# Performance work log

Measured on AMD Instinct MI355X. Metric: run time of the kernel, lower is better.

The kernel has to match this reference:

```python
import jax, jax.numpy as jnp
import numpy as np

LAG = 5
MSG_HID = 256
N_ATOMS = 30
N_EDGES = N_ATOMS * (N_ATOMS - 1)  # 870
BATCH = 2
T = 200


def _rel_matrices():
    # fully-connected directed graph, no self loops (standard NRI encoding)
    recv, send = [], []
    for i in range(N_ATOMS):
        for j in range(N_ATOMS):
            if i != j:
                recv.append(i)
                send.append(j)
    rel_rec = np.zeros((N_EDGES, N_ATOMS), dtype=np.float32)
    rel_send = np.zeros((N_EDGES, N_ATOMS), dtype=np.float32)
    rel_rec[np.arange(N_EDGES), recv] = 1.0
    rel_send[np.arange(N_EDGES), send] = 1.0
    return jnp.asarray(rel_rec), jnp.asarray(rel_send)


def setup_inputs() -> dict:
    key = jax.random.key(0)
    ks = jax.random.split(key, 14)
    rel_rec, rel_send = _rel_matrices()
    s = 0.05
    return {
        "inputs": jax.random.normal(ks[0], (BATCH, N_ATOMS, T), jnp.float32),
        "mu": jax.random.normal(ks[1], (BATCH, N_EDGES), jnp.float32),
        "logvar": jax.random.normal(ks[2], (BATCH, N_EDGES), jnp.float32) * 0.1,
        "eps": jax.random.normal(ks[3], (BATCH, N_EDGES), jnp.float32),
        "rel_rec": rel_rec,
        "rel_send": rel_send,
        "w_msg1": jax.random.normal(ks[4], (2 * LAG, MSG_HID), jnp.float32) * s,
        "b_msg1": jnp.zeros((MSG_HID,), jnp.float32),
        "w_msg2": jax.random.normal(ks[5], (MSG_HID, MSG_HID), jnp.float32) * s,
        "b_msg2": jnp.zeros((MSG_HID,), jnp.float32),
        "w_out1": jax.random.normal(ks[6], (LAG + MSG_HID, MSG_HID), jnp.float32) * s,
        "b_out1": jnp.zeros((MSG_HID,), jnp.float32),
        "w_out2": jax.random.normal(ks[7], (MSG_HID, MSG_HID), jnp.float32) * s,
        "b_out2": jnp.zeros((MSG_HID,), jnp.float32),
        "w_out3": jax.random.normal(ks[8], (MSG_HID, 1), jnp.float32) * s,
        "b_out3": jnp.zeros((1,), jnp.float32),
    }


def reference(inputs, mu, logvar, eps, rel_rec, rel_send,
              w_msg1, b_msg1, w_msg2, b_msg2,
              w_out1, b_out1, w_out2, b_out2, w_out3, b_out3):
    # reparametrize: edges [B, E]
    edges = eps * jnp.exp(0.5 * logvar) + mu

    # lag-stack: data [B, T-lag, N, lag]
    Tm = inputs.shape[2] - LAG
    data = jnp.stack([inputs[:, :, i:i + Tm] for i in range(LAG)], axis=-1)
    data = jnp.transpose(data, (0, 2, 1, 3))  # [B, Tm, N, lag]

    # gather node features to edges via one-hot matmuls
    receivers = jnp.einsum('en,btnl->btel', rel_rec, data)   # [B, Tm, E, lag]
    senders = jnp.einsum('en,btnl->btel', rel_send, data)    # [B, Tm, E, lag]
    pre_msg = jnp.concatenate([senders, receivers], axis=-1)  # [B, Tm, E, 2*lag]

    msg = jax.nn.relu(pre_msg @ w_msg1 + b_msg1)
    msg = jax.nn.relu(msg @ w_msg2 + b_msg2)                 # [B, Tm, E, hid]
    msg = msg * edges[:, None, :, None]                       # edge mask

    # scatter-aggregate messages back to receiver nodes
    agg_msgs = jnp.einsum('bteh,en->btnh', msg, rel_rec)      # [B, Tm, N, hid]

    aug = jnp.concatenate([data, agg_msgs], axis=-1)          # [B, Tm, N, lag+hid]
    pred = jax.nn.relu(aug @ w_out1 + b_out1)
    pred = jax.nn.relu(pred @ w_out2 + b_out2)
    pred = (pred @ w_out3 + b_out3)[..., 0]                   # [B, Tm, N]

    return jnp.transpose(pred, (0, 2, 1))                     # [B, N, Tm]
```

## Files before the change

kernel.cpp:

```cpp
#include <hip/hip_runtime.h>

#define LAG 5
#define HID 256
#define NA 30
#define NE 870
#define TM 195
#define TT 200
#define NB 2
#define EPN 29
#define TB2 98
#define NROWS (NB * TM * NA)
#define APAD 4
#define KC 32
#define UVSLABS (NB * TM)
#define W2F_ELEMS (HID * HID)
#define W1F_ELEMS (HID * 288)
#define NWG2 (NB * NA * TB2)
#define Q8 (NWG2 / 8)

typedef _Float16 f16;
typedef _Float16 f16x8 __attribute__((ext_vector_type(8)));
typedef float floatx4 __attribute__((ext_vector_type(4)));
typedef float floatx16 __attribute__((ext_vector_type(16)));

__global__ __launch_bounds__(256) void k1_prep(
    const float* __restrict__ inputs, const float* __restrict__ w_msg1,
    const float* __restrict__ b_msg1, const float* __restrict__ w_msg2,
    const float* __restrict__ w_out1, const float* __restrict__ w_out2,
    f16* __restrict__ u, f16* __restrict__ v, f16* __restrict__ w2frag,
    f16* __restrict__ w1frag, f16* __restrict__ w2ofrag)
{
    const int bid = blockIdx.x, tid = threadIdx.x;
    if (bid < UVSLABS) {
        __shared__ float w1_lds[10 * 256];
        __shared__ float b1_lds[256];
        __shared__ float feats[30 * 5];
        const int b = bid / TM, t = bid % TM;
        #pragma unroll
        for (int i = 0; i < 10; ++i) w1_lds[i * 256 + tid] = w_msg1[i * 256 + tid];
        b1_lds[tid] = b_msg1[tid];
        if (tid < 150) {
            const int n = tid / 5, l = tid % 5;
            feats[tid] = inputs[(b * NA + n) * TT + t + l];
        }
        __syncthreads();
        if (tid < 240) {
            const int n = tid >> 3;
            float fr[LAG];
            #pragma unroll
            for (int l = 0; l < LAG; ++l) fr[l] = feats[n * 5 + l];
            const int slab = (b * TM + t) * (32 * 240);
            #pragma unroll 4
            for (int c = 0; c < 32; ++c) {
                const int col = c * 8 + (tid & 7);
                float ua = b1_lds[col], va = 0.f;
                #pragma unroll
                for (int l = 0; l < LAG; ++l) {
                    ua = fmaf(fr[l], w1_lds[l * 256 + col], ua);
                    va = fmaf(fr[l], w1_lds[(LAG + l) * 256 + col], va);
                }
                u[slab + c * 240 + tid] = (f16)ua;
                v[slab + c * 240 + tid] = (f16)va;
            }
        }
    } else if (bid < UVSLABS + 32) {
        const int fidx = (bid - UVSLABS) * 256 + tid;
        const int lane = fidx & 63;
        const int kc = (fidx >> 6) & 15;
        const int c32 = fidx >> 10;
        const int col = c32 * 32 + (lane & 31);
        const int kb = kc * 16 + (lane >> 5) * 8;
        f16x8 vv;
        #pragma unroll
        for (int x = 0; x < 8; ++x) vv[x] = (f16)w_msg2[(kb + x) * HID + col];
        *(f16x8*)&w2frag[fidx * 8] = vv;
    } else if (bid < UVSLABS + 32 + 36) {
        const int fidx = (bid - (UVSLABS + 32)) * 256 + tid;
        const int lane = fidx & 63;
        const int kc = (fidx >> 6) % 9;
        const int ntc = fidx / (64 * 9);
        const int col = ntc * 16 + (lane & 15);
        const int kb = kc * KC + (lane >> 4) * 8;
        f16x8 vv;
        #pragma unroll
        for (int x = 0; x < 8; ++x) {
            const int k = kb + x;
            float val;
            if (k < 256)      val = w_out1[(5 + k) * HID + col];
            else if (k < 261) val = w_out1[(k - 256) * HID + col];
            else              val = 0.f;
            vv[x] = (f16)val;
        }
        *(f16x8*)&w1frag[fidx * 8] = vv;
    } else {
        const int fidx = (bid - (UVSLABS + 32 + 36)) * 256 + tid;
        const int lane = fidx & 63;
        const int kc = (fidx >> 6) & 7;
        const int ntc = fidx >> 9;
        const int col = ntc * 16 + (lane & 15);
        const int kb = kc * KC + (lane >> 4) * 8;
        f16x8 vv;
        #pragma unroll
        for (int x = 0; x < 8; ++x) vv[x] = (f16)w_out2[(kb + x) * HID + col];
        *(f16x8*)&w2ofrag[fidx * 8] = vv;
    }
}

__global__ __launch_bounds__(256, 4) void k2_msg(
    const f16* __restrict__ u, const f16* __restrict__ v,
    const f16* __restrict__ w2frag,
    const float* __restrict__ mu, const float* __restrict__ logvar,
    const float* __restrict__ eps, const float* __restrict__ b_msg2,
    f16* __restrict__ agg)
{
    __shared__ f16 a_lds[32 * 64 * 8];
    __shared__ float ev_lds[32];

    const int bid0 = blockIdx.x;
    const int bid = (bid0 & 7) * Q8 + (bid0 >> 3);

    const int n  = bid % NA;
    const int tb = (bid / NA) % TB2;
    const int b  = bid / (NA * TB2);
    const int t0 = tb * 2;
    const int tid = threadIdx.x;
    const int lane = tid & 63, w = tid >> 6;
    const int h = lane >> 5, l31 = lane & 31;

    if (tid < 32) {
        float evv = 0.f;
        if (tid < EPN) {
            const int e = b * NE + n * EPN + tid;
            evv = eps[e] * __expf(0.5f * logvar[e]) + mu[e];
        }
        ev_lds[tid] = evv;
    }

    const f16x8 z8 = {(f16)0, (f16)0, (f16)0, (f16)0, (f16)0, (f16)0, (f16)0, (f16)0};

    auto stage_iter = [&](int i) {
        const int task = i * 256 + tid;
        const int frag = task >> 6, fl = task & 63;
        const int tt = frag >> 4, kcs = frag & 15;
        const int hh = fl >> 5, ei = fl & 31;
        const int c = kcs * 2 + hh;
        const int t = t0 + tt;
        f16x8 out8 = z8;
        if (ei < EPN && t < TM) {
            const int rowbase = ((b * TM + t) * 32 + c) * 240;
            const int j = ei + (ei >= n);
            const f16x8 uu = *(const f16x8*)(u + rowbase + j * 8);
            const f16x8 vv = *(const f16x8*)(v + rowbase + n * 8);
            out8 = __builtin_elementwise_max(uu + vv, z8);
        }
        *(f16x8*)&a_lds[task * 8] = out8;
    };

    #pragma unroll
    for (int s = 0; s < 4; ++s) stage_iter(s < 2 ? s : s + 2);

    const f16* bb[2];
    bb[0] = w2frag + (((2 * w + 0) * 16) << 9) + (lane << 3);
    bb[1] = w2frag + (((2 * w + 1) * 16) << 9) + (lane << 3);
    f16x8 b0[2], b1[2];
    #pragma unroll
    for (int nt = 0; nt < 2; ++nt) {
        b0[nt] = *(const f16x8*)(bb[nt] + (0 << 9));
        b1[nt] = *(const f16x8*)(bb[nt] + (1 << 9));
    }

    floatx16 acc[2][2];
    #pragma unroll
    for (int tt = 0; tt < 2; ++tt)
        #pragma unroll
        for (int nt = 0; nt < 2; ++nt)
            #pragma unroll
            for (int x = 0; x < 16; ++x) acc[tt][nt][x] = 0.f;

    __syncthreads();

    #pragma unroll
    for (int kc = 0; kc < 8; ++kc) {
        f16x8 b2[2];
        #pragma unroll
        for (int nt = 0; nt < 2; ++nt)
            b2[nt] = *(const f16x8*)(bb[nt] + ((kc + 2) << 9));
        f16x8 af[2];
        #pragma unroll
        for (int tt = 0; tt < 2; ++tt)
            af[tt] = *(const f16x8*)&a_lds[((tt * 16 + kc) * 64 + lane) * 8];
        __builtin_amdgcn_s_setprio(1);
        #pragma unroll
        for (int nt = 0; nt < 2; ++nt)
            #pragma unroll
            for (int tt = 0; tt < 2; ++tt)
                acc[tt][nt] = __builtin_amdgcn_mfma_f32_32x32x16_f16(af[tt], b0[nt], acc[tt][nt], 0, 0, 0);
        __builtin_amdgcn_s_setprio(0);
        #pragma unroll
        for (int nt = 0; nt < 2; ++nt) { b0[nt] = b1[nt]; b1[nt] = b2[nt]; }
        if ((kc & 1) == 0) {
            const int half = kc >> 1;
            stage_iter(half < 2 ? half + 2 : half + 4);
        }
    }

    __syncthreads();

    #pragma unroll
    for (int kc = 8; kc < 16; ++kc) {
        f16x8 b2[2];
        #pragma unroll
        for (int nt = 0; nt < 2; ++nt) {
            b2[nt] = b1[nt];
            if (kc < 14) b2[nt] = *(const f16x8*)(bb[nt] + ((kc + 2) << 9));
        }
        f16x8 af[2];
        #pragma unroll
        for (int tt = 0; tt < 2; ++tt)
            af[tt] = *(const f16x8*)&a_lds[((tt * 16 + kc) * 64 + lane) * 8];
        __builtin_amdgcn_s_setprio(1);
        #pragma unroll
        for (int nt = 0; nt < 2; ++nt)
            #pragma unroll
            for (int tt = 0; tt < 2; ++tt)
                acc[tt][nt] = __builtin_amdgcn_mfma_f32_32x32x16_f16(af[tt], b0[nt], acc[tt][nt], 0, 0, 0);
        __builtin_amdgcn_s_setprio(0);
        #pragma unroll
        for (int nt = 0; nt < 2; ++nt) { b0[nt] = b1[nt]; b1[nt] = b2[nt]; }
    }

    float evr[16];
    #pragma unroll
    for (int reg = 0; reg < 16; ++reg)
        evr[reg] = ev_lds[(reg & 3) + 8 * (reg >> 2) + 4 * h];
    float b2s[2];
    #pragma unroll
    for (int nt = 0; nt < 2; ++nt) b2s[nt] = b_msg2[(2 * w + nt) * 32 + l31];

    #pragma unroll
    for (int tt = 0; tt < 2; ++tt) {
        const int t = t0 + tt;
        #pragma unroll
        for (int nt = 0; nt < 2; ++nt) {
            float part = 0.f;
            #pragma unroll
            for (int reg = 0; reg < 16; ++reg)
                part += evr[reg] * fmaxf(acc[tt][nt][reg] + b2s[nt], 0.f);
            part += __shfl_xor(part, 32, 64);
            if (h == 0 && t < TM)
                agg[(((b * TM + t) * NA + n) << 8) + (2 * w + nt) * 32 + l31] = (f16)part;
        }
    }
}

__global__ __launch_bounds__(256) void k3_out(
    const f16* __restrict__ agg, const float* __restrict__ inputs,
    const f16* __restrict__ w1frag, const f16* __restrict__ w2ofrag,
    const float* __restrict__ b_out1, const float* __restrict__ b_out2,
    const float* __restrict__ w_out3, const float* __restrict__ b_out3,
    float* __restrict__ out)
{
    __shared__ f16 a1[32][288 + APAD];
    __shared__ float red[4][32];

    const int R0 = blockIdx.x * 32;
    const int tid = threadIdx.x;
    const int lane = tid & 63, w = tid >> 6;
    const int q = lane >> 4, m15 = lane & 15;
    const int wbase = w * 64;

    #pragma unroll
    for (int i = 0; i < 4; ++i) {
        const int task = i * 256 + tid;
        const int row = task >> 5, c = task & 31;
        const int R = R0 + row;
        f16x8 val;
        if (R < NROWS) {
            val = *(const f16x8*)&agg[(R << 8) + c * 8];
        } else {
            for (int x = 0; x < 8; ++x) val[x] = (f16)0.f;
        }
        *(f16x8*)&a1[row][c * 8] = val;
    }
    if (tid < 32) {
        const int R = R0 + tid;
        if (R < NROWS) {
            const int b = R / (TM * NA), rem = R % (TM * NA);
            const int t = rem / NA, n = rem % NA;
            const float* ip = inputs + (b * NA + n) * TT + t;
            #pragma unroll
            for (int l = 0; l < LAG; ++l) a1[tid][256 + l] = (f16)ip[l];
            #pragma unroll
            for (int k = 261; k < 288; ++k) a1[tid][k] = (f16)0.f;
        } else {
            for (int k = 256; k < 288; ++k) a1[tid][k] = (f16)0.f;
        }
    }

    floatx4 acc[2][4];
    #pragma unroll
    for (int ms = 0; ms < 2; ++ms)
        #pragma unroll
        for (int nt = 0; nt < 4; ++nt) acc[ms][nt] = (floatx4){0.f, 0.f, 0.f, 0.f};

    const f16* b1base = w1frag + (lane << 3);
    f16x8 bcur[4], bnxt[4];
    #pragma unroll
    for (int nt = 0; nt < 4; ++nt)
        bcur[nt] = *(const f16x8*)(b1base + (((w * 4 + nt) * 9 + 0) << 9));

    __syncthreads();

    #pragma unroll
    for (int kc = 0; kc < 9; ++kc) {
        if (kc < 8) {
            #pragma unroll
            for (int nt = 0; nt < 4; ++nt)
                bnxt[nt] = *(const f16x8*)(b1base + (((w * 4 + nt) * 9 + kc + 1) << 9));
        }
        f16x8 af[2];
        #pragma unroll
        for (int ms = 0; ms < 2; ++ms)
            af[ms] = *(const f16x8*)&a1[ms * 16 + m15][kc * KC + q * 8];
        #pragma unroll
        for (int nt = 0; nt < 4; ++nt)
            #pragma unroll
            for (int ms = 0; ms < 2; ++ms)
                acc[ms][nt] = __builtin_amdgcn_mfma_f32_16x16x32_f16(af[ms], bcur[nt], acc[ms][nt], 0, 0, 0);
        #pragma unroll
        for (int nt = 0; nt < 4; ++nt) bcur[nt] = bnxt[nt];
    }
    __syncthreads();

    {
        float b1v[4];
        #pragma unroll
        for (int nt = 0; nt < 4; ++nt) b1v[nt] = b_out1[wbase + nt * 16 + m15];
        #pragma unroll
        for (int ms = 0; ms < 2; ++ms)
            #pragma unroll
            for (int nt = 0; nt < 4; ++nt)
                #pragma unroll
                for (int reg = 0; reg < 4; ++reg)
                    a1[ms * 16 + q * 4 + reg][wbase + nt * 16 + m15] =
                        (f16)fmaxf(acc[ms][nt][reg] + b1v[nt], 0.f);
    }

    #pragma unroll
    for (int ms = 0; ms < 2; ++ms)
        #pragma unroll
        for (int nt = 0; nt < 4; ++nt) acc[ms][nt] = (floatx4){0.f, 0.f, 0.f, 0.f};

    const f16* b2base = w2ofrag + (lane << 3);
    #pragma unroll
    for (int nt = 0; nt < 4; ++nt)
        bcur[nt] = *(const f16x8*)(b2base + (((w * 4 + nt) * 8 + 0) << 9));

    __syncthreads();

    #pragma unroll
    for (int kc = 0; kc < 8; ++kc) {
        if (kc < 7) {
            #pragma unroll
            for (int nt = 0; nt < 4; ++nt)
                bnxt[nt] = *(const f16x8*)(b2base + (((w * 4 + nt) * 8 + kc + 1) << 9));
        }
        f16x8 af[2];
        #pragma unroll
        for (int ms = 0; ms < 2; ++ms)
            af[ms] = *(const f16x8*)&a1[ms * 16 + m15][kc * KC + q * 8];
        #pragma unroll
        for (int nt = 0; nt < 4; ++nt)
            #pragma unroll
            for (int ms = 0; ms < 2; ++ms)
                acc[ms][nt] = __builtin_amdgcn_mfma_f32_16x16x32_f16(af[ms], bcur[nt], acc[ms][nt], 0, 0, 0);
        #pragma unroll
        for (int nt = 0; nt < 4; ++nt) bcur[nt] = bnxt[nt];
    }

    {
        float b2v[4], w3v[4];
        #pragma unroll
        for (int nt = 0; nt < 4; ++nt) {
            const int col = wbase + nt * 16 + m15;
            b2v[nt] = b_out2[col];
            w3v[nt] = w_out3[col];
        }
        #pragma unroll
        for (int ms = 0; ms < 2; ++ms)
            #pragma unroll
            for (int reg = 0; reg < 4; ++reg) {
                float p = 0.f;
                #pragma unroll
                for (int nt = 0; nt < 4; ++nt)
                    p += fmaxf(acc[ms][nt][reg] + b2v[nt], 0.f) * w3v[nt];
                p += __shfl_xor(p, 1, 64);
                p += __shfl_xor(p, 2, 64);
                p += __shfl_xor(p, 4, 64);
                p += __shfl_xor(p, 8, 64);
                if (m15 == 0) red[w][ms * 16 + q * 4 + reg] = p;
            }
    }
    __syncthreads();
    if (tid < 32) {
        const int R = R0 + tid;
        if (R < NROWS) {
            const float val = red[0][tid] + red[1][tid] + red[2][tid] + red[3][tid] + b_out3[0];
            const int b = R / (TM * NA), rem = R % (TM * NA);
            const int t = rem / NA, n = rem % NA;
            out[(b * NA + n) * TM + t] = val;
        }
    }
}

extern "C" void kernel_launch(void* const* d_in, const int* in_sizes, int n_in,
                              void* d_out, int out_size, void* d_ws, size_t ws_size,
                              hipStream_t stream) {
    const float* inputs  = (const float*)d_in[0];
    const float* mu      = (const float*)d_in[1];
    const float* logvar  = (const float*)d_in[2];
    const float* eps     = (const float*)d_in[3];
    const float* w_msg1  = (const float*)d_in[6];
    const float* b_msg1  = (const float*)d_in[7];
    const float* w_msg2  = (const float*)d_in[8];
    const float* b_msg2  = (const float*)d_in[9];
    const float* w_out1  = (const float*)d_in[10];
    const float* b_out1  = (const float*)d_in[11];
    const float* w_out2  = (const float*)d_in[12];
    const float* b_out2  = (const float*)d_in[13];
    const float* w_out3  = (const float*)d_in[14];
    const float* b_out3  = (const float*)d_in[15];
    float* out = (float*)d_out;

    f16* u       = (f16*)d_ws;
    f16* v       = u       + NROWS * HID;
    f16* aggw    = v       + NROWS * HID;
    f16* w2frag  = aggw    + NROWS * HID;
    f16* w1frag  = w2frag  + W2F_ELEMS;
    f16* w2ofrag = w1frag  + W1F_ELEMS;

    hipLaunchKernelGGL(k1_prep, dim3(UVSLABS + 32 + 36 + 32), dim3(256), 0, stream,
                       inputs, w_msg1, b_msg1, w_msg2, w_out1, w_out2,
                       u, v, w2frag, w1frag, w2ofrag);
    hipLaunchKernelGGL(k2_msg, dim3(NWG2), dim3(256), 0, stream,
                       u, v, w2frag, mu, logvar, eps, b_msg2, aggw);
    hipLaunchKernelGGL(k3_out, dim3((NROWS + 31) / 32), dim3(256), 0, stream,
                       aggw, inputs, w1frag, w2ofrag, b_out1, b_out2, w_out3, b_out3, out);
}
```

Before: 165.0 us.

## Widen k2 message workgroups to four timesteps with eight waves

The message kernel now processes four timesteps per workgroup with 512 threads. Waves are split 2x4 over timestep pairs and output column blocks, so each W2 fragment load from global memory is reused across more rows and the grid has half as many workgroups. The staging of the A tile into LDS is no longer interleaved with the first half of the MFMA loop; all of it is done up front behind a single barrier. Edge weights are broadcast with a wave shuffle instead of an LDS array, and the XCD block remapping now handles a grid size that is not a multiple of eight. The trade-off is doubled LDS per workgroup (64 KB) and fewer workgroups, which may reduce occupancy, and the staging latency is no longer hidden behind compute.

Measured after the change: 168.3 us. No clear change (+2.0%).

```diff
diff --git a/kernel.cpp b/kernel.cpp
--- a/kernel.cpp
+++ b/kernel.cpp
@@ -8,15 +8,16 @@
 #define TT 200
 #define NB 2
 #define EPN 29
-#define TB2 98
+#define TB4 49
 #define NROWS (NB * TM * NA)
 #define APAD 4
 #define KC 32
 #define UVSLABS (NB * TM)
 #define W2F_ELEMS (HID * HID)
 #define W1F_ELEMS (HID * 288)
-#define NWG2 (NB * NA * TB2)
+#define NWG2 (NB * NA * TB4)
 #define Q8 (NWG2 / 8)
+#define R8 (NWG2 % 8)
 
 typedef _Float16 f16;
 typedef _Float16 f16x8 __attribute__((ext_vector_type(8)));
@@ -106,40 +107,39 @@
     }
 }
 
-__global__ __launch_bounds__(256, 4) void k2_msg(
+__global__ __launch_bounds__(512, 4) void k2_msg(
     const f16* __restrict__ u, const f16* __restrict__ v,
     const f16* __restrict__ w2frag,
     const float* __restrict__ mu, const float* __restrict__ logvar,
     const float* __restrict__ eps, const float* __restrict__ b_msg2,
     f16* __restrict__ agg)
 {
-    __shared__ f16 a_lds[32 * 64 * 8];
-    __shared__ float ev_lds[32];
+    __shared__ f16 a_lds[64 * 64 * 8];
 
     const int bid0 = blockIdx.x;
-    const int bid = (bid0 & 7) * Q8 + (bid0 >> 3);
+    const int xcd = bid0 & 7, sub = bid0 >> 3;
+    const int bid = (xcd < R8 ? xcd * (Q8 + 1) : R8 * (Q8 + 1) + (xcd - R8) * Q8) + sub;
 
     const int n  = bid % NA;
-    const int tb = (bid / NA) % TB2;
-    const int b  = bid / (NA * TB2);
-    const int t0 = tb * 2;
+    const int tb = (bid / NA) % TB4;
+    const int b  = bid / (NA * TB4);
+    const int t0 = tb * 4;
     const int tid = threadIdx.x;
     const int lane = tid & 63, w = tid >> 6;
+    const int wm = w & 1, wn = w >> 1;
     const int h = lane >> 5, l31 = lane & 31;
 
-    if (tid < 32) {
-        float evv = 0.f;
-        if (tid < EPN) {
-            const int e = b * NE + n * EPN + tid;
-            evv = eps[e] * __expf(0.5f * logvar[e]) + mu[e];
-        }
-        ev_lds[tid] = evv;
+    float evfull = 0.f;
+    if (l31 < EPN) {
+        const int e = b * NE + n * EPN + l31;
+        evfull = eps[e] * __expf(0.5f * logvar[e]) + mu[e];
     }
 
     const f16x8 z8 = {(f16)0, (f16)0, (f16)0, (f16)0, (f16)0, (f16)0, (f16)0, (f16)0};
 
-    auto stage_iter = [&](int i) {
-        const int task = i * 256 + tid;
+    #pragma unroll
+    for (int i = 0; i < 8; ++i) {
+        const int task = i * 512 + tid;
         const int frag = task >> 6, fl = task & 63;
         const int tt = frag >> 4, kcs = frag & 15;
         const int hh = fl >> 5, ei = fl & 31;
@@ -154,14 +154,11 @@
             out8 = __builtin_elementwise_max(uu + vv, z8);
         }
         *(f16x8*)&a_lds[task * 8] = out8;
-    };
-
-    #pragma unroll
-    for (int s = 0; s < 4; ++s) stage_iter(s < 2 ? s : s + 2);
+    }
 
     const f16* bb[2];
-    bb[0] = w2frag + (((2 * w + 0) * 16) << 9) + (lane << 3);
-    bb[1] = w2frag + (((2 * w + 1) * 16) << 9) + (lane << 3);
+    bb[0] = w2frag + (((2 * wn + 0) * 16) << 9) + (lane << 3);
+    bb[1] = w2frag + (((2 * wn + 1) * 16) << 9) + (lane << 3);
     f16x8 b0[2], b1[2];
     #pragma unroll
     for (int nt = 0; nt < 2; ++nt) {
@@ -171,43 +168,16 @@
 
     floatx16 acc[2][2];
     #pragma unroll
-    for (int tt = 0; tt < 2; ++tt)
+    for (int t2 = 0; t2 < 2; ++t2)
         #pragma unroll
         for (int nt = 0; nt < 2; ++nt)
             #pragma unroll
-            for (int x = 0; x < 16; ++x) acc[tt][nt][x] = 0.f;
+            for (int x = 0; x < 16; ++x) acc[t2][nt][x] = 0.f;
 
     __syncthreads();
 
     #pragma unroll
-    for (int kc = 0; kc < 8; ++kc) {
-        f16x8 b2[2];
-        #pragma unroll
-        for (int nt = 0; nt < 2; ++nt)
-            b2[nt] = *(const f16x8*)(bb[nt] + ((kc + 2) << 9));
-        f16x8 af[2];
-        #pragma unroll
-        for (int tt = 0; tt < 2; ++tt)
-            af[tt] = *(const f16x8*)&a_lds[((tt * 16 + kc) * 64 + lane) * 8];
-        __builtin_amdgcn_s_setprio(1);
-        #pragma unroll
-        for (int nt = 0; nt < 2; ++nt)
-            #pragma unroll
-            for (int tt = 0; tt < 2; ++tt)
-                acc[tt][nt] = __builtin_amdgcn_mfma_f32_32x32x16_f16(af[tt], b0[nt], acc[tt][nt], 0, 0, 0);
-        __builtin_amdgcn_s_setprio(0);
-        #pragma unroll
-        for (int nt = 0; nt < 2; ++nt) { b0[nt] = b1[nt]; b1[nt] = b2[nt]; }
-        if ((kc & 1) == 0) {
-            const int half = kc >> 1;
-            stage_iter(half < 2 ? half + 2 : half + 4);
-        }
-    }
-
-    __syncthreads();
-
-    #pragma unroll
-    for (int kc = 8; kc < 16; ++kc) {
+    for (int kc = 0; kc < 16; ++kc) {
         f16x8 b2[2];
         #pragma unroll
         for (int nt = 0; nt < 2; ++nt) {
@@ -216,14 +186,14 @@
         }
         f16x8 af[2];
         #pragma unroll
-        for (int tt = 0; tt < 2; ++tt)
-            af[tt] = *(const f16x8*)&a_lds[((tt * 16 + kc) * 64 + lane) * 8];
+        for (int t2 = 0; t2 < 2; ++t2)
+            af[t2] = *(const f16x8*)&a_lds[(((wm * 2 + t2) * 16 + kc) * 64 + lane) * 8];
         __builtin_amdgcn_s_setprio(1);
         #pragma unroll
         for (int nt = 0; nt < 2; ++nt)
             #pragma unroll
-            for (int tt = 0; tt < 2; ++tt)
-                acc[tt][nt] = __builtin_amdgcn_mfma_f32_32x32x16_f16(af[tt], b0[nt], acc[tt][nt], 0, 0, 0);
+            for (int t2 = 0; t2 < 2; ++t2)
+                acc[t2][nt] = __builtin_amdgcn_mfma_f32_32x32x16_f16(af[t2], b0[nt], acc[t2][nt], 0, 0, 0);
         __builtin_amdgcn_s_setprio(0);
         #pragma unroll
         for (int nt = 0; nt < 2; ++nt) { b0[nt] = b1[nt]; b1[nt] = b2[nt]; }
@@ -232,23 +202,23 @@
     float evr[16];
     #pragma unroll
     for (int reg = 0; reg < 16; ++reg)
-        evr[reg] = ev_lds[(reg & 3) + 8 * (reg >> 2) + 4 * h];
+        evr[reg] = __shfl(evfull, (reg & 3) + 8 * (reg >> 2) + 4 * h, 64);
     float b2s[2];
     #pragma unroll
-    for (int nt = 0; nt < 2; ++nt) b2s[nt] = b_msg2[(2 * w + nt) * 32 + l31];
-
-    #pragma unroll
-    for (int tt = 0; tt < 2; ++tt) {
-        const int t = t0 + tt;
+    for (int nt = 0; nt < 2; ++nt) b2s[nt] = b_msg2[(2 * wn + nt) * 32 + l31];
+
+    #pragma unroll
+    for (int t2 = 0; t2 < 2; ++t2) {
+        const int t = t0 + wm * 2 + t2;
         #pragma unroll
         for (int nt = 0; nt < 2; ++nt) {
             float part = 0.f;
             #pragma unroll
             for (int reg = 0; reg < 16; ++reg)
-                part += evr[reg] * fmaxf(acc[tt][nt][reg] + b2s[nt], 0.f);
+                part += evr[reg] * fmaxf(acc[t2][nt][reg] + b2s[nt], 0.f);
             part += __shfl_xor(part, 32, 64);
             if (h == 0 && t < TM)
-                agg[(((b * TM + t) * NA + n) << 8) + (2 * w + nt) * 32 + l31] = (f16)part;
+                agg[(((b * TM + t) * NA + n) << 8) + (2 * wn + nt) * 32 + l31] = (f16)part;
         }
     }
 }
@@ -442,7 +412,7 @@
     hipLaunchKernelGGL(k1_prep, dim3(UVSLABS + 32 + 36 + 32), dim3(256), 0, stream,
                        inputs, w_msg1, b_msg1, w_msg2, w_out1, w_out2,
                        u, v, w2frag, w1frag, w2ofrag);
-    hipLaunchKernelGGL(k2_msg, dim3(NWG2), dim3(256), 0, stream,
+    hipLaunchKernelGGL(k2_msg, dim3(NWG2), dim3(512), 0, stream,
                        u, v, w2frag, mu, logvar, eps, b_msg2, aggw);
     hipLaunchKernelGGL(k3_out, dim3((NROWS + 31) / 32), dim3(256), 0, stream,
                        aggw, inputs, w1frag, w2ofrag, b_out1, b_out2, w_out3, b_out3, out);
```

## Make k2_msg persistent with W2 fragments held in registers

Applied to the files above, without the earlier changes.

Changes k2_msg from one workgroup per (batch, time-pair, node) tile to a persistent grid of 512 workgroups that loop over tiles. Each wave loads all its w_msg2 MFMA fragments into registers once and reuses them across tiles, instead of streaming them from global memory for every tile. This costs more VGPRs, so occupancy is lowered to 2 waves per SIMD. The earlier overlap of staging with MFMA and the XCD-aware block swizzle are removed, so staging now runs serially before the MFMA loop in each tile.

Result: slower. 171.1 us (+3.7%).

```diff
diff --git a/kernel.cpp b/kernel.cpp
--- a/kernel.cpp
+++ b/kernel.cpp
@@ -15,8 +15,8 @@
 #define UVSLABS (NB * TM)
 #define W2F_ELEMS (HID * HID)
 #define W1F_ELEMS (HID * 288)
-#define NWG2 (NB * NA * TB2)
-#define Q8 (NWG2 / 8)
+#define NTILES2 (NB * TB2 * NA)
+#define K2GRID 512
 
 typedef _Float16 f16;
 typedef _Float16 f16x8 __attribute__((ext_vector_type(8)));
@@ -106,7 +106,7 @@
     }
 }
 
-__global__ __launch_bounds__(256, 4) void k2_msg(
+__global__ __launch_bounds__(256, 2) void k2_msg(
     const f16* __restrict__ u, const f16* __restrict__ v,
     const f16* __restrict__ w2frag,
     const float* __restrict__ mu, const float* __restrict__ logvar,
@@ -116,139 +116,101 @@
     __shared__ f16 a_lds[32 * 64 * 8];
     __shared__ float ev_lds[32];
 
-    const int bid0 = blockIdx.x;
-    const int bid = (bid0 & 7) * Q8 + (bid0 >> 3);
-
-    const int n  = bid % NA;
-    const int tb = (bid / NA) % TB2;
-    const int b  = bid / (NA * TB2);
-    const int t0 = tb * 2;
     const int tid = threadIdx.x;
     const int lane = tid & 63, w = tid >> 6;
     const int h = lane >> 5, l31 = lane & 31;
 
-    if (tid < 32) {
-        float evv = 0.f;
-        if (tid < EPN) {
-            const int e = b * NE + n * EPN + tid;
-            evv = eps[e] * __expf(0.5f * logvar[e]) + mu[e];
-        }
-        ev_lds[tid] = evv;
-    }
+    f16x8 bfr[2][16];
+    #pragma unroll
+    for (int nt = 0; nt < 2; ++nt)
+        #pragma unroll
+        for (int kc = 0; kc < 16; ++kc)
+            bfr[nt][kc] = *(const f16x8*)(w2frag + ((((2 * w + nt) * 16 + kc) << 9) + (lane << 3)));
+
+    float b2s[2];
+    #pragma unroll
+    for (int nt = 0; nt < 2; ++nt) b2s[nt] = b_msg2[(2 * w + nt) * 32 + l31];
 
     const f16x8 z8 = {(f16)0, (f16)0, (f16)0, (f16)0, (f16)0, (f16)0, (f16)0, (f16)0};
 
-    auto stage_iter = [&](int i) {
-        const int task = i * 256 + tid;
-        const int frag = task >> 6, fl = task & 63;
-        const int tt = frag >> 4, kcs = frag & 15;
-        const int hh = fl >> 5, ei = fl & 31;
-        const int c = kcs * 2 + hh;
-        const int t = t0 + tt;
-        f16x8 out8 = z8;
-        if (ei < EPN && t < TM) {
-            const int rowbase = ((b * TM + t) * 32 + c) * 240;
-            const int j = ei + (ei >= n);
-            const f16x8 uu = *(const f16x8*)(u + rowbase + j * 8);
-            const f16x8 vv = *(const f16x8*)(v + rowbase + n * 8);
-            out8 = __builtin_elementwise_max(uu + vv, z8);
-        }
-        *(f16x8*)&a_lds[task * 8] = out8;
-    };
-
-    #pragma unroll
-    for (int s = 0; s < 4; ++s) stage_iter(s < 2 ? s : s + 2);
-
-    const f16* bb[2];
-    bb[0] = w2frag + (((2 * w + 0) * 16) << 9) + (lane << 3);
-    bb[1] = w2frag + (((2 * w + 1) * 16) << 9) + (lane << 3);
-    f16x8 b0[2], b1[2];
-    #pragma unroll
-    for (int nt = 0; nt < 2; ++nt) {
-        b0[nt] = *(const f16x8*)(bb[nt] + (0 << 9));
-        b1[nt] = *(const f16x8*)(bb[nt] + (1 << 9));
-    }
-
-    floatx16 acc[2][2];
-    #pragma unroll
-    for (int tt = 0; tt < 2; ++tt)
-        #pragma unroll
-        for (int nt = 0; nt < 2; ++nt)
-            #pragma unroll
-            for (int x = 0; x < 16; ++x) acc[tt][nt][x] = 0.f;
-
-    __syncthreads();
-
-    #pragma unroll
-    for (int kc = 0; kc < 8; ++kc) {
-        f16x8 b2[2];
-        #pragma unroll
-        for (int nt = 0; nt < 2; ++nt)
-            b2[nt] = *(const f16x8*)(bb[nt] + ((kc + 2) << 9));
-        f16x8 af[2];
+    for (int tile = blockIdx.x; tile < NTILES2; tile += K2GRID) {
+        const int n  = tile % NA;
+        const int tb = (tile / NA) % TB2;
+        const int b  = tile / (NA * TB2);
+        const int t0 = tb * 2;
+
+        __syncthreads();
+
+        #pragma unroll
+        for (int i = 0; i < 8; ++i) {
+            const int task = i * 256 + tid;
+            const int frag = task >> 6, fl = task & 63;
+            const int tt = frag >> 4, kcs = frag & 15;
+            const int hh = fl >> 5, ei = fl & 31;
+            const int c = kcs * 2 + hh;
+            const int t = t0 + tt;
+            f16x8 out8 = z8;
+            if (ei < EPN && t < TM) {
+                const int rowbase = ((b * TM + t) * 32 + c) * 240;
+                const int j = ei + (ei >= n);
+                const f16x8 uu = *(const f16x8*)(u + rowbase + j * 8);
+                const f16x8 vv = *(const f16x8*)(v + rowbase + n * 8);
+                out8 = __builtin_elementwise_max(uu + vv, z8);
+            }
+            *(f16x8*)&a_lds[task * 8] = out8;
+        }
+        if (tid < 32) {
+            float evv = 0.f;
+            if (tid < EPN) {
+                const int e = b * NE + n * EPN + tid;
+                evv = eps[e] * __expf(0.5f * logvar[e]) + mu[e];
+            }
+            ev_lds[tid] = evv;
+        }
+
+        floatx16 acc[2][2];
         #pragma unroll
         for (int tt = 0; tt < 2; ++tt)
-            af[tt] = *(const f16x8*)&a_lds[((tt * 16 + kc) * 64 + lane) * 8];
+            #pragma unroll
+            for (int nt = 0; nt < 2; ++nt)
+                #pragma unroll
+                for (int x = 0; x < 16; ++x) acc[tt][nt][x] = 0.f;
+
+        __syncthreads();
+
         __builtin_amdgcn_s_setprio(1);
         #pragma unroll
-        for (int nt = 0; nt < 2; ++nt)
+        for (int kc = 0; kc < 16; ++kc) {
+            f16x8 af[2];
             #pragma unroll
             for (int tt = 0; tt < 2; ++tt)
-                acc[tt][nt] = __builtin_amdgcn_mfma_f32_32x32x16_f16(af[tt], b0[nt], acc[tt][nt], 0, 0, 0);
+                af[tt] = *(const f16x8*)&a_lds[((tt * 16 + kc) * 64 + lane) * 8];
+            #pragma unroll
+            for (int nt = 0; nt < 2; ++nt)
+                #pragma unroll
+                for (int tt = 0; tt < 2; ++tt)
+                    acc[tt][nt] = __builtin_amdgcn_mfma_f32_32x32x16_f16(af[tt], bfr[nt][kc], acc[tt][nt], 0, 0, 0);
+        }
         __builtin_amdgcn_s_setprio(0);
-        #pragma unroll
-        for (int nt = 0; nt < 2; ++nt) { b0[nt] = b1[nt]; b1[nt] = b2[nt]; }
-        if ((kc & 1) == 0) {
-            const int half = kc >> 1;
-            stage_iter(half < 2 ? half + 2 : half + 4);
-        }
-    }
-
-    __syncthreads();
-
-    #pragma unroll
-    for (int kc = 8; kc < 16; ++kc) {
-        f16x8 b2[2];
-        #pragma unroll
-        for (int nt = 0; nt < 2; ++nt) {
-            b2[nt] = b1[nt];
-            if (kc < 14) b2[nt] = *(const f16x8*)(bb[nt] + ((kc + 2) << 9));
-        }
-        f16x8 af[2];
-        #pragma unroll
-        for (int tt = 0; tt < 2; ++tt)
-            af[tt] = *(const f16x8*)&a_lds[((tt * 16 + kc) * 64 + lane) * 8];
-        __builtin_amdgcn_s_setprio(1);
-        #pragma unroll
-        for (int nt = 0; nt < 2; ++nt)
-            #pragma unroll
-            for (int tt = 0; tt < 2; ++tt)
-                acc[tt][nt] = __builtin_amdgcn_mfma_f32_32x32x16_f16(af[tt], b0[nt], acc[tt][nt], 0, 0, 0);
-        __builtin_amdgcn_s_setprio(0);
-        #pragma unroll
-        for (int nt = 0; nt < 2; ++nt) { b0[nt] = b1[nt]; b1[nt] = b2[nt]; }
-    }
-
-    float evr[16];
-    #pragma unroll
-    for (int reg = 0; reg < 16; ++reg)
-        evr[reg] = ev_lds[(reg & 3) + 8 * (reg >> 2) + 4 * h];
-    float b2s[2];
-    #pragma unroll
-    for (int nt = 0; nt < 2; ++nt) b2s[nt] = b_msg2[(2 * w + nt) * 32 + l31];
-
-    #pragma unroll
-    for (int tt = 0; tt < 2; ++tt) {
-        const int t = t0 + tt;
-        #pragma unroll
-        for (int nt = 0; nt < 2; ++nt) {
-            float part = 0.f;
-            #pragma unroll
-            for (int reg = 0; reg < 16; ++reg)
-                part += evr[reg] * fmaxf(acc[tt][nt][reg] + b2s[nt], 0.f);
-            part += __shfl_xor(part, 32, 64);
-            if (h == 0 && t < TM)
-                agg[(((b * TM + t) * NA + n) << 8) + (2 * w + nt) * 32 + l31] = (f16)part;
+
+        float evr[16];
+        #pragma unroll
+        for (int reg = 0; reg < 16; ++reg)
+            evr[reg] = ev_lds[(reg & 3) + 8 * (reg >> 2) + 4 * h];
+
+        #pragma unroll
+        for (int tt = 0; tt < 2; ++tt) {
+            const int t = t0 + tt;
+            #pragma unroll
+            for (int nt = 0; nt < 2; ++nt) {
+                float part = 0.f;
+                #pragma unroll
+                for (int reg = 0; reg < 16; ++reg)
+                    part += evr[reg] * fmaxf(acc[tt][nt][reg] + b2s[nt], 0.f);
+                part += __shfl_xor(part, 32, 64);
+                if (h == 0 && t < TM)
+                    agg[(((b * TM + t) * NA + n) << 8) + (2 * w + nt) * 32 + l31] = (f16)part;
+            }
         }
     }
 }
@@ -442,7 +404,7 @@
     hipLaunchKernelGGL(k1_prep, dim3(UVSLABS + 32 + 36 + 32), dim3(256), 0, stream,
                        inputs, w_msg1, b_msg1, w_msg2, w_out1, w_out2,
                        u, v, w2frag, w1frag, w2ofrag);
-    hipLaunchKernelGGL(k2_msg, dim3(NWG2), dim3(256), 0, stream,
+    hipLaunchKernelGGL(k2_msg, dim3(K2GRID), dim3(256), 0, stream,
                        u, v, w2frag, mu, logvar, eps, b_msg2, aggw);
     hipLaunchKernelGGL(k3_out, dim3((NROWS + 31) / 32), dim3(256), 0, stream,
                        aggw, inputs, w1frag, w2ofrag, b_out1, b_out2, w_out3, b_out3, out);
```
